# Kernel optimization log

Hardware: AMD Instinct MI355X
Metric: run time of the kernel (lower is better)

Reference implementation:

```python
import jax, jax.numpy as jnp
import numpy as np

E, NL, CH, M1, M2 = 8, 4, 32, 16, 16   # experts, fno layers, hidden channels, fourier modes
HD, NH, NENC = 64, 4, 2                 # router hidden dim, heads, encoder layers
B, CIN, H, W, COUT = 32, 1, 128, 128, 1
PCH = 128                               # projection channels


def _ln(h, s, b):
    mu = h.mean(-1, keepdims=True)
    v = ((h - mu) ** 2).mean(-1, keepdims=True)
    return (h - mu) / jnp.sqrt(v + 1e-5) * s + b


def _router(x, enc_in_w, enc_in_b, qkv_w, qkv_b, ao_w, ao_b,
            ln1_s, ln1_b, ff1_w, ff1_b, ff2_w, ff2_b, ln2_s, ln2_b, fc_w, fc_b):
    ic = x[:, :, 0, :]                                        # (B, C, W): initial condition
    h = jnp.einsum('bcs,cd->bsd', ic, enc_in_w) + enc_in_b    # (B, S, HD)
    S = h.shape[1]
    dh = HD // NH
    for l in range(NENC):  # small fixed layer count
        qkv = h @ qkv_w[l] + qkv_b[l]
        q, k, v = jnp.split(qkv, 3, axis=-1)
        q = q.reshape(-1, S, NH, dh)
        k = k.reshape(-1, S, NH, dh)
        v = v.reshape(-1, S, NH, dh)
        att = jax.nn.softmax(jnp.einsum('bqhd,bkhd->bhqk', q, k) / np.float32(np.sqrt(dh)), axis=-1)
        o = jnp.einsum('bhqk,bkhd->bqhd', att, v).reshape(-1, S, HD)
        h = _ln(h + o @ ao_w[l] + ao_b[l], ln1_s[l], ln1_b[l])
        ff = jax.nn.relu(h @ ff1_w[l] + ff1_b[l]) @ ff2_w[l] + ff2_b[l]
        h = _ln(h + ff, ln2_s[l], ln2_b[l])
    feats = h.mean(axis=1)                                    # (B, HD)
    logits = feats @ fc_w + fc_b                              # (B, E)
    return jnp.argmax(logits, axis=-1), logits                # hard routing (eval path)


def _fno(x, idx, lift_w, lift_b, spec_wr, spec_wi, skip_w, skip_b, p1_w, p1_b, p2_w, p2_b):
    # Hard-MoE dispatch/combine expressed as per-sample expert-weight gather:
    # mathematically identical to running each sample through its selected expert.
    v = jnp.einsum('bchw,bcd->bdhw', x, lift_w[idx]) + lift_b[idx][:, :, None, None]
    for l in range(NL):
        Wc = spec_wr[idx, l] + 1j * spec_wi[idx, l]           # (B,2,CH,CH,M1,M2) complex
        X = jnp.fft.rfft2(v)                                  # (B,CH,H,W//2+1)
        o1 = jnp.einsum('bixy,bioxy->boxy', X[:, :, :M1, :M2], Wc[:, 0])
        o2 = jnp.einsum('bixy,bioxy->boxy', X[:, :, -M1:, :M2], Wc[:, 1])
        out_ft = jnp.zeros(X.shape, X.dtype).at[:, :, :M1, :M2].set(o1).at[:, :, -M1:, :M2].set(o2)
        spec = jnp.fft.irfft2(out_ft, s=(v.shape[-2], v.shape[-1]))
        skip = jnp.einsum('bihw,bio->bohw', v, skip_w[idx, l]) + skip_b[idx, l][:, :, None, None]
        v = spec + skip
        if l < NL - 1:
            v = jax.nn.gelu(v)
    h = jax.nn.gelu(jnp.einsum('bihw,bio->bohw', v, p1_w[idx]) + p1_b[idx][:, :, None, None])
    return jnp.einsum('bihw,bio->bohw', h, p2_w[idx]) + p2_b[idx][:, :, None, None]


def setup_inputs() -> dict:
    key = jax.random.key(0)
    ks = iter(jax.random.split(key, 40))
    def rn(shape, scale=1.0):
        return jax.random.normal(next(ks), shape, jnp.float32) * scale
    return {
        'x': rn((B, CIN, H, W)),
        'enc_in_w': rn((CIN, HD)), 'enc_in_b': jnp.zeros((HD,), jnp.float32),
        'qkv_w': rn((NENC, HD, 3 * HD), HD ** -0.5), 'qkv_b': jnp.zeros((NENC, 3 * HD), jnp.float32),
        'ao_w': rn((NENC, HD, HD), HD ** -0.5), 'ao_b': jnp.zeros((NENC, HD), jnp.float32),
        'ln1_s': jnp.ones((NENC, HD), jnp.float32), 'ln1_b': jnp.zeros((NENC, HD), jnp.float32),
        'ff1_w': rn((NENC, HD, 4 * HD), HD ** -0.5), 'ff1_b': jnp.zeros((NENC, 4 * HD), jnp.float32),
        'ff2_w': rn((NENC, 4 * HD, HD), (4 * HD) ** -0.5), 'ff2_b': jnp.zeros((NENC, HD), jnp.float32),
        'ln2_s': jnp.ones((NENC, HD), jnp.float32), 'ln2_b': jnp.zeros((NENC, HD), jnp.float32),
        'fc_w': rn((HD, E), HD ** -0.5), 'fc_b': jnp.zeros((E,), jnp.float32),
        'lift_w': rn((E, CIN, CH)), 'lift_b': jnp.zeros((E, CH), jnp.float32),
        'spec_wr': rn((E, NL, 2, CH, CH, M1, M2), 1.0 / CH),
        'spec_wi': rn((E, NL, 2, CH, CH, M1, M2), 1.0 / CH),
        'skip_w': rn((E, NL, CH, CH), CH ** -0.5), 'skip_b': jnp.zeros((E, NL, CH), jnp.float32),
        'p1_w': rn((E, CH, PCH), CH ** -0.5), 'p1_b': jnp.zeros((E, PCH), jnp.float32),
        'p2_w': rn((E, PCH, COUT), PCH ** -0.5), 'p2_b': jnp.zeros((E, COUT), jnp.float32),
    }


def reference(x, enc_in_w, enc_in_b, qkv_w, qkv_b, ao_w, ao_b, ln1_s, ln1_b,
              ff1_w, ff1_b, ff2_w, ff2_b, ln2_s, ln2_b, fc_w, fc_b,
              lift_w, lift_b, spec_wr, spec_wi, skip_w, skip_b, p1_w, p1_b, p2_w, p2_b):
    idx, _ = _router(x, enc_in_w, enc_in_b, qkv_w, qkv_b, ao_w, ao_b,
                     ln1_s, ln1_b, ff1_w, ff1_b, ff2_w, ff2_b, ln2_s, ln2_b, fc_w, fc_b)
    return _fno(x, idx, lift_w, lift_b, spec_wr, spec_wi, skip_w, skip_b, p1_w, p1_b, p2_w, p2_b)
```

## Files before the change

kernel.cpp:

```cpp
#include <hip/hip_runtime.h>
#include <hip/hip_bf16.h>
#include <math.h>

typedef __attribute__((ext_vector_type(8))) short bf16x8;
typedef __attribute__((ext_vector_type(4))) float f32x4;
typedef __attribute__((ext_vector_type(2))) float f32x2;

__device__ __forceinline__ float gelu_f(float x){
    float u = 0.7978845608028654f*(x + 0.044715f*x*x*x);
    float e = __expf(2.0f*u);
    float th = 1.0f - 2.0f/(e + 1.0f);
    return 0.5f*x*(1.0f + th);
}

__device__ __forceinline__ short f2bs(float f){
    unsigned u = __float_as_uint(f);
    u += 0x7FFF + ((u>>16)&1);
    return (short)(u>>16);
}

__global__ void r_embed(const float* __restrict__ x, const float* __restrict__ ew,
                        const float* __restrict__ eb, float* __restrict__ h){
    int t = blockIdx.x*256 + threadIdx.x;
    int d = t & 63, s = (t>>6)&127, b = t>>13;
    h[t] = x[b*16384 + s]*ew[d] + eb[d];
}

__global__ void r_qkv(const float* __restrict__ h, const float* __restrict__ w,
                      const float* __restrict__ bias, int woff, int boff,
                      float* __restrict__ qkv){
    int t = blockIdx.x*256 + threadIdx.x;
    int j = t % 192; int sb = t/192;
    const float* hr = h + sb*64;
    float acc = bias[boff + j];
    #pragma unroll
    for(int d=0; d<64; ++d) acc += hr[d]*w[woff + d*192 + j];
    qkv[t] = acc;
}

__global__ __launch_bounds__(128) void r_attn(const float* __restrict__ qkv,
                                              float* __restrict__ o){
    __shared__ float Ks[128][16];
    __shared__ float Vs[128][16];
    int b  = blockIdx.x >> 2;
    int hd = blockIdx.x & 3;
    int q  = threadIdx.x;
    const float* base = qkv + b*128*192;
    {
        const float* kr = base + q*192 + 64  + hd*16;
        const float* vr = base + q*192 + 128 + hd*16;
        #pragma unroll
        for(int j=0;j<4;++j){
            *(float4*)&Ks[q][4*j] = *(const float4*)(kr + 4*j);
            *(float4*)&Vs[q][4*j] = *(const float4*)(vr + 4*j);
        }
    }
    float qv[16];
    {
        const float* qr = base + q*192 + hd*16;
        #pragma unroll
        for(int d=0;d<16;++d) qv[d] = qr[d];
    }
    __syncthreads();
    float m = -1e30f;
    #pragma unroll 4
    for(int k=0;k<128;++k){
        float acc=0.f;
        #pragma unroll
        for(int d=0;d<16;++d) acc += qv[d]*Ks[k][d];
        m = fmaxf(m, acc*0.25f);
    }
    float sum=0.f; float ov[16];
    #pragma unroll
    for(int d=0;d<16;++d) ov[d]=0.f;
    #pragma unroll 2
    for(int k=0;k<128;++k){
        float acc=0.f;
        #pragma unroll
        for(int d=0;d<16;++d) acc += qv[d]*Ks[k][d];
        float p = __expf(acc*0.25f - m); sum += p;
        #pragma unroll
        for(int d=0;d<16;++d) ov[d] += p*Vs[k][d];
    }
    float inv = 1.0f/sum;
    float* orow = o + (b*128+q)*64 + hd*16;
    #pragma unroll
    for(int d=0;d<16;++d) orow[d] = ov[d]*inv;
}

__global__ void r_proj_res(const float* __restrict__ h, const float* __restrict__ o,
                           const float* __restrict__ w, const float* __restrict__ bias,
                           int woff, int boff, float* __restrict__ r){
    int t = blockIdx.x*256 + threadIdx.x;
    int d = t & 63; int sb = t>>6;
    const float* orow = o + sb*64;
    float acc = bias[boff + d];
    #pragma unroll
    for(int e=0;e<64;++e) acc += orow[e]*w[woff + e*64 + d];
    r[t] = h[t] + acc;
}

__global__ void r_ln(const float* __restrict__ r, const float* __restrict__ s,
                     const float* __restrict__ bias, int off, float* __restrict__ h){
    int row = blockIdx.x*64 + threadIdx.x;
    const float* rr = r + row*64;
    float mu=0.f;
    #pragma unroll
    for(int d=0;d<64;++d) mu += rr[d];
    mu *= (1.0f/64.0f);
    float var=0.f;
    #pragma unroll
    for(int d=0;d<64;++d){ float df = rr[d]-mu; var += df*df; }
    var *= (1.0f/64.0f);
    float inv = rsqrtf(var + 1e-5f);
    float* hr = h + row*64;
    #pragma unroll
    for(int d=0;d<64;++d) hr[d] = (rr[d]-mu)*inv*s[off+d] + bias[off+d];
}

__global__ void r_ffn(const float* __restrict__ h, const float* __restrict__ w1,
                      const float* __restrict__ b1, const float* __restrict__ w2,
                      const float* __restrict__ b2,
                      int w1off, int b1off, int w2off, int b2off,
                      float* __restrict__ r){
    __shared__ float hrow[64];
    __shared__ float uval[256];
    int row = blockIdx.x;
    int tid = threadIdx.x;
    if(tid < 64) hrow[tid] = h[row*64 + tid];
    __syncthreads();
    {
        float acc = b1[b1off + tid];
        #pragma unroll
        for(int d=0; d<64; ++d) acc += hrow[d]*w1[w1off + d*256 + tid];
        uval[tid] = fmaxf(acc, 0.0f);
    }
    __syncthreads();
    if(tid < 64){
        float acc = b2[b2off + tid];
        for(int j=0;j<256;++j) acc += uval[j]*w2[w2off + j*64 + tid];
        r[row*64 + tid] = hrow[tid] + acc;
    }
}

__global__ void r_head(const float* __restrict__ h, const float* __restrict__ fcw,
                       const float* __restrict__ fcb, int* __restrict__ idx){
    __shared__ float feats[64];
    __shared__ float lg[8];
    int b = blockIdx.x; int d = threadIdx.x;
    float acc=0.f;
    for(int s2=0;s2<128;++s2) acc += h[(b*128+s2)*64 + d];
    feats[d] = acc*(1.0f/128.0f);
    __syncthreads();
    if(d<8){
        float a = fcb[d];
        for(int e=0;e<64;++e) a += feats[e]*fcw[e*8+d];
        lg[d]=a;
    }
    __syncthreads();
    if(d==0){
        int best=0; float bv=lg[0];
        for(int e=1;e<8;++e) if(lg[e]>bv){bv=lg[e];best=e;}
        idx[b]=best;
    }
}

__global__ void f_lift(const float* __restrict__ x, const float* __restrict__ lw,
                       const float* __restrict__ lb, const int* __restrict__ idx,
                       int b0, float* __restrict__ v){
    int t = blockIdx.x*256 + threadIdx.x;
    int w = t & 127; int h2 = (t>>7)&127; int d = (t>>14)&31; int bl = t>>19;
    int b = b0 + bl;
    int e = idx[b];
    v[t] = x[b*16384 + h2*128 + w]*lw[e*32+d] + lb[e*32+d];
}

__global__ __launch_bounds__(256) void f_fwd(const float* __restrict__ v,
                                             float* __restrict__ G){
    __shared__ float cT[128], sT[128];
    __shared__ float X[2*16*260 + 8];
    int tid = threadIdx.x;
    if(tid<128){ float sv,cv; __sincosf(6.283185307179586f*tid/128.0f,&sv,&cv); cT[tid]=cv; sT[tid]=sv; }
    __syncthreads();
    int bi0 = blockIdx.x*2;
    {
        int bil = tid>>7, h = tid&127;
        const float* row = v + ((bi0+bil)*128 + h)*128;
        float Xr[16], Xi[16];
        #pragma unroll
        for(int k=0;k<16;++k){ Xr[k]=0.f; Xi[k]=0.f; }
        #pragma unroll
        for(int j=0;j<8;++j){
            float4 a = *(const float4*)(row + 4*j);
            float4 bq= *(const float4*)(row + 4*j + 32);
            float4 c = *(const float4*)(row + 4*j + 64);
            float4 dq= *(const float4*)(row + 4*j + 96);
            #pragma unroll
            for(int r=0;r<4;++r){
                int g = 4*j + r;
                float va = (r==0)?a.x:(r==1)?a.y:(r==2)?a.z:a.w;
                float vb = (r==0)?bq.x:(r==1)?bq.y:(r==2)?bq.z:bq.w;
                float vc = (r==0)?c.x:(r==1)?c.y:(r==2)?c.z:c.w;
                float vd = (r==0)?dq.x:(r==1)?dq.y:(r==2)?dq.z:dq.w;
                float s1=va+vc, s2=vb+vd, d1=va-vc, d2=vb-vd;
                float rsum=s1+s2, rdif=s1-s2;
                float pc=cT[g], ps=-sT[g];
                float cr=1.f, ci=0.f;
                #pragma unroll
                for(int ky=0;ky<16;++ky){
                    int mm = ky&3;
                    if(mm==0){ Xr[ky]+=cr*rsum; Xi[ky]+=ci*rsum; }
                    else if(mm==1){ Xr[ky]+=cr*d1+ci*d2; Xi[ky]+=ci*d1-cr*d2; }
                    else if(mm==2){ Xr[ky]+=cr*rdif; Xi[ky]+=ci*rdif; }
                    else { Xr[ky]+=cr*d1-ci*d2; Xi[ky]+=ci*d1+cr*d2; }
                    float tt=cr*pc-ci*ps; ci=cr*ps+ci*pc; cr=tt;
                }
            }
        }
        float* Xb = X + bil*4160;
        #pragma unroll
        for(int ky=0;ky<16;++ky){
            Xb[ky*260 + h*2]   = Xr[ky];
            Xb[ky*260 + h*2+1] = Xi[ky];
        }
    }
    __syncthreads();
    {
        int ky = tid&15, kg = (tid>>4)&7, bil = tid>>7;
        int bi = bi0 + bil;
        const float* Xb = X + bil*4160 + ky*260;
        int kxs[4] = {kg, kg+8, kg+112, kg+120};
        float qc[4], qs[4];
        #pragma unroll
        for(int m2=0;m2<4;++m2){ qc[m2]=cT[kxs[m2]&127]; qs[m2]=-sT[kxs[m2]&127]; }
        float cr[4]={1.f,1.f,1.f,1.f}, ci[4]={0.f,0.f,0.f,0.f};
        float Gr[4]={0.f,0.f,0.f,0.f}, Gi[4]={0.f,0.f,0.f,0.f};
        for(int h=0;h<128;++h){
            float Xr=Xb[h*2], Xi2=Xb[h*2+1];
            #pragma unroll
            for(int m2=0;m2<4;++m2){
                Gr[m2] += Xr*cr[m2] - Xi2*ci[m2];
                Gi[m2] += Xr*ci[m2] + Xi2*cr[m2];
                float t=cr[m2]*qc[m2]-ci[m2]*qs[m2]; ci[m2]=cr[m2]*qs[m2]+ci[m2]*qc[m2]; cr[m2]=t;
            }
        }
        #pragma unroll
        for(int m2=0;m2<4;++m2){
            int kxi = kg + 8*m2;
            G[((bi*32+kxi)*16+ky)*2]   = Gr[m2];
            G[((bi*32+kxi)*16+ky)*2+1] = Gi[m2];
        }
    }
}

__global__ void f_specmul(const float* __restrict__ G, const float* __restrict__ wr,
                          const float* __restrict__ wi, const int* __restrict__ idx,
                          int l, int b0, float* __restrict__ Go){
    int t = blockIdx.x*256 + threadIdx.x;
    int ky = t & 15; int kxi = (t>>4)&31; int o = (t>>9)&31; int bl = t>>14;
    int e = __builtin_amdgcn_readfirstlane(idx[b0 + bl]);
    int side = (kxi>=16) ? 1 : 0; int xm = kxi & 15;
    int wbase = ((((e*4+l)*2+side)*32)*32 + o)*256 + xm*16 + ky;
    const float* gp = G + ((bl*1024 + kxi)*16 + ky)*2;
    float orr=0.f, oii=0.f;
    #pragma unroll 8
    for(int i=0;i<32;++i){
        float gr = gp[i*1024], gi = gp[i*1024+1];
        float wrv = wr[wbase + i*8192];
        float wiv = wi[wbase + i*8192];
        orr += gr*wrv - gi*wiv;
        oii += gr*wiv + gi*wrv;
    }
    Go[t*2]=orr; Go[t*2+1]=oii;
}

__global__ __launch_bounds__(128) void f_idft_h(const float* __restrict__ Go,
                                                float* __restrict__ T){
    __shared__ float cT[128], sT[128];
    int tid = threadIdx.x;
    { float sv,cv; __sincosf(6.283185307179586f*tid/128.0f,&sv,&cv); cT[tid]=cv; sT[tid]=sv; }
    __syncthreads();
    int bo = blockIdx.x;
    const float* g = Go + bo*1024;
    int h = tid;
    float Mc = cT[h], Ms = sT[h];
    float Tr[16], Ti[16];
    #pragma unroll
    for(int k=0;k<16;++k){ Tr[k]=0.f; Ti[k]=0.f; }
    {   float cr=1.f, ci=0.f;
        for(int kxi=0;kxi<16;++kxi){
            #pragma unroll
            for(int ky=0;ky<16;++ky){
                float gr=g[(kxi*16+ky)*2], gi=g[(kxi*16+ky)*2+1];
                Tr[ky] += gr*cr - gi*ci;
                Ti[ky] += gr*ci + gi*cr;
            }
            float t=cr*Mc-ci*Ms; ci=cr*Ms+ci*Mc; cr=t;
        }
    }
    {   float cr=1.f, ci=0.f;
        for(int m=1;m<=16;++m){
            float t=cr*Mc+ci*Ms; ci=ci*Mc-cr*Ms; cr=t;
            int kxi = 32 - m;
            #pragma unroll
            for(int ky=0;ky<16;++ky){
                float gr=g[(kxi*16+ky)*2], gi=g[(kxi*16+ky)*2+1];
                Tr[ky] += gr*cr - gi*ci;
                Ti[ky] += gr*ci + gi*cr;
            }
        }
    }
    float* out = T + (bo*128 + h)*32;
    #pragma unroll
    for(int k=0;k<8;++k){
        *(float4*)(out + 4*k) = make_float4(Tr[2*k], Ti[2*k], Tr[2*k+1], Ti[2*k+1]);
    }
}

__global__ __launch_bounds__(128) void f_inv_w_skip(const float* __restrict__ T,
                             float* __restrict__ v,
                             const float* __restrict__ skw, const float* __restrict__ skb,
                             const int* __restrict__ idx, int l, int act, int b0){
    __shared__ float Tl[1024];
    __shared__ float Wl[1024];
    int tid = threadIdx.x;
    int bl = blockIdx.x >> 7; int h2 = blockIdx.x & 127;
    int e = __builtin_amdgcn_readfirstlane(idx[b0 + bl]);
    int w = tid;
    const float* swp = skw + (e*4+l)*1024;
    const float* sbp = skb + (e*4+l)*32;
    {
        #pragma unroll
        for(int rep=0; rep<2; ++rep){
            int g = rep*512 + tid*4;
            int o = g>>5, j = g&31;
            *(float4*)&Tl[g] = *(const float4*)(T + ((bl*32+o)*128 + h2)*32 + j);
        }
        int gi = tid>>2, go = (tid&3)*8;
        float4 wa = *(const float4*)(swp + gi*32 + go);
        float4 wb = *(const float4*)(swp + gi*32 + go + 4);
        Wl[(go+0)*32+gi]=wa.x; Wl[(go+1)*32+gi]=wa.y;
        Wl[(go+2)*32+gi]=wa.z; Wl[(go+3)*32+gi]=wa.w;
        Wl[(go+4)*32+gi]=wb.x; Wl[(go+5)*32+gi]=wb.y;
        Wl[(go+6)*32+gi]=wb.z; Wl[(go+7)*32+gi]=wb.w;
    }
    f32x2 vv[16];
    #pragma unroll
    for(int i=0;i<16;++i){
        float lo = v[((bl*32+2*i  )*128+h2)*128 + w];
        float hi = v[((bl*32+2*i+1)*128+h2)*128 + w];
        vv[i].x = lo; vv[i].y = hi;
    }
    f32x2 CS[16];
    {
        float bs, bc; __sincosf(6.283185307179586f*w/128.0f, &bs, &bc);
        float cr=bc, ci=bs;
        CS[0].x = 1.f; CS[0].y = 0.f;
        #pragma unroll
        for(int ky=1;ky<16;++ky){
            CS[ky].x = 2.f*cr; CS[ky].y = -2.f*ci;
            float t2=cr*bc-ci*bs; ci=cr*bs+ci*bc; cr=t2;
        }
    }
    __syncthreads();
    #pragma unroll 1
    for(int o=0;o<32;o+=2){
        const f32x2* W0 = (const f32x2*)&Wl[o*32];
        const f32x2* W1 = (const f32x2*)&Wl[o*32+32];
        const f32x2* T0 = (const f32x2*)&Tl[o*32];
        const f32x2* T1 = (const f32x2*)&Tl[o*32+32];
        f32x2 a  = {0.f,0.f}, a2 = {0.f,0.f};
        f32x2 b  = {0.f,0.f}, b2 = {0.f,0.f};
        f32x2 s  = {0.f,0.f}, s2 = {0.f,0.f};
        f32x2 t  = {0.f,0.f}, t2 = {0.f,0.f};
        #pragma unroll
        for(int k=0;k<16;k+=2){
            a  = vv[k]  *W0[k]   + a;
            a2 = vv[k+1]*W0[k+1] + a2;
            b  = vv[k]  *W1[k]   + b;
            b2 = vv[k+1]*W1[k+1] + b2;
            s  = T0[k]  *CS[k]   + s;
            s2 = T0[k+1]*CS[k+1] + s2;
            t  = T1[k]  *CS[k]   + t;
            t2 = T1[k+1]*CS[k+1] + t2;
        }
        float skip0 = sbp[o]   + ((a.x+a.y)+(a2.x+a2.y));
        float skip1 = sbp[o+1] + ((b.x+b.y)+(b2.x+b2.y));
        float spec0 = (s.x+s.y)+(s2.x+s2.y);
        float spec1 = (t.x+t.y)+(t2.x+t2.y);
        float val0 = spec0*(1.0f/16384.0f) + skip0;
        float val1 = spec1*(1.0f/16384.0f) + skip1;
        if(act){ val0 = gelu_f(val0); val1 = gelu_f(val1); }
        v[((bl*32+o  )*128+h2)*128 + w] = val0;
        v[((bl*32+o+1)*128+h2)*128 + w] = val1;
    }
}

__global__ __launch_bounds__(256) void f_proj(const float* __restrict__ vin,
                       const float* __restrict__ p1w, const float* __restrict__ p1b,
                       const float* __restrict__ p2w, const float* __restrict__ p2b,
                       const int* __restrict__ idx, int b0, float* __restrict__ out){
    int tid = threadIdx.x;
    int wv  = tid>>6, lane = tid&63;
    int blk = blockIdx.x;
    int bl  = blk>>5; int part = blk&31;
    int b   = b0 + bl;
    int e   = __builtin_amdgcn_readfirstlane(idx[b]);
    int m   = lane&15, quad = lane>>4;
    const float* w1 = p1w + e*4096;
    bf16x8 bfr[8]; float b1v[8], w2v[8];
    #pragma unroll
    for(int og=0; og<8; ++og){
        int o = og*16 + m;
        #pragma unroll
        for(int j=0;j<8;++j){
            int k = quad*8 + j;
            bfr[og][j] = f2bs(w1[k*128 + o]);
        }
        b1v[og] = p1b[e*128+o];
        w2v[og] = p2w[e*128+o];
    }
    float p2bv = p2b[e];
    const float* vbase = vin + (size_t)bl*524288;
    for(int t=0;t<8;++t){
        int tile = part*32 + wv*8 + t;
        int pix0 = tile*16;
        bf16x8 af;
        #pragma unroll
        for(int j=0;j<8;++j){
            int k = quad*8 + j;
            af[j] = f2bs(vbase[k*16384 + pix0 + m]);
        }
        float acc0=0.f, acc1=0.f, acc2=0.f, acc3=0.f;
        #pragma unroll
        for(int og=0;og<8;++og){
            f32x4 d = {0.f,0.f,0.f,0.f};
            d = __builtin_amdgcn_mfma_f32_16x16x32_bf16(af, bfr[og], d, 0,0,0);
            acc0 += w2v[og]*gelu_f(d[0]+b1v[og]);
            acc1 += w2v[og]*gelu_f(d[1]+b1v[og]);
            acc2 += w2v[og]*gelu_f(d[2]+b1v[og]);
            acc3 += w2v[og]*gelu_f(d[3]+b1v[og]);
        }
        #pragma unroll
        for(int s=1;s<16;s<<=1){
            acc0 += __shfl_xor(acc0, s, 64);
            acc1 += __shfl_xor(acc1, s, 64);
            acc2 += __shfl_xor(acc2, s, 64);
            acc3 += __shfl_xor(acc3, s, 64);
        }
        if(m==0){
            int pix = pix0 + quad*4;
            *(float4*)(out + (size_t)b*16384 + pix) =
                make_float4(acc0+p2bv, acc1+p2bv, acc2+p2bv, acc3+p2bv);
        }
    }
}

extern "C" void kernel_launch(void* const* d_in, const int* in_sizes, int n_in,
                              void* d_out, int out_size, void* d_ws, size_t ws_size,
                              hipStream_t stream){
    const float* x      = (const float*)d_in[0];
    const float* enc_w  = (const float*)d_in[1];
    const float* enc_b  = (const float*)d_in[2];
    const float* qkv_w  = (const float*)d_in[3];
    const float* qkv_b  = (const float*)d_in[4];
    const float* ao_w   = (const float*)d_in[5];
    const float* ao_b   = (const float*)d_in[6];
    const float* ln1_s  = (const float*)d_in[7];
    const float* ln1_b  = (const float*)d_in[8];
    const float* ff1_w  = (const float*)d_in[9];
    const float* ff1_b  = (const float*)d_in[10];
    const float* ff2_w  = (const float*)d_in[11];
    const float* ff2_b  = (const float*)d_in[12];
    const float* ln2_s  = (const float*)d_in[13];
    const float* ln2_b  = (const float*)d_in[14];
    const float* fc_w   = (const float*)d_in[15];
    const float* fc_b   = (const float*)d_in[16];
    const float* lift_w = (const float*)d_in[17];
    const float* lift_b = (const float*)d_in[18];
    const float* spec_wr= (const float*)d_in[19];
    const float* spec_wi= (const float*)d_in[20];
    const float* skip_w = (const float*)d_in[21];
    const float* skip_b = (const float*)d_in[22];
    const float* p1_w   = (const float*)d_in[23];
    const float* p1_b   = (const float*)d_in[24];
    const float* p2_w   = (const float*)d_in[25];
    const float* p2_b   = (const float*)d_in[26];

    int*   idx   = (int*)d_ws + 8;
    float* base  = (float*)d_ws + 64;

    size_t avail_fl = (ws_size/4 > 64) ? (ws_size/4 - 64) : 0;
    int nb = 1;
    for(int c = 32; c >= 1; c >>= 1){
        if((size_t)c*851968 <= avail_fl){ nb = c; break; }
    }

    float* hbuf  = base;
    float* qkvb  = hbuf + 262144;
    float* obuf  = qkvb + 786432;
    float* rbuf  = obuf + 262144;

    r_embed<<<1024,256,0,stream>>>(x, enc_w, enc_b, hbuf);
    for(int l=0;l<2;++l){
        r_qkv<<<3072,256,0,stream>>>(hbuf, qkv_w, qkv_b, l*64*192, l*192, qkvb);
        r_attn<<<128,128,0,stream>>>(qkvb, obuf);
        r_proj_res<<<1024,256,0,stream>>>(hbuf, obuf, ao_w, ao_b, l*64*64, l*64, rbuf);
        r_ln<<<64,64,0,stream>>>(rbuf, ln1_s, ln1_b, l*64, hbuf);
        r_ffn<<<4096,256,0,stream>>>(hbuf, ff1_w, ff1_b, ff2_w, ff2_b,
                                     l*64*256, l*256, l*256*64, l*64, rbuf);
        r_ln<<<64,64,0,stream>>>(rbuf, ln2_s, ln2_b, l*64, hbuf);
    }
    r_head<<<32,64,0,stream>>>(hbuf, fc_w, fc_b, idx);

    for(int b0 = 0; b0 < 32; b0 += nb){
        float* vC = base;
        float* G  = vC + (size_t)nb*655360;
        float* Go = G  + (size_t)nb*32768;
        float* T  = Go + (size_t)nb*32768;

        f_lift<<<nb*2048,256,0,stream>>>(x, lift_w, lift_b, idx, b0, vC);
        for(int l=0;l<4;++l){
            f_fwd    <<<nb*16, 256,0,stream>>>(vC, G);
            f_specmul<<<nb*64, 256,0,stream>>>(G, spec_wr, spec_wi, idx, l, b0, Go);
            f_idft_h <<<nb*32, 128,0,stream>>>(Go, T);
            f_inv_w_skip<<<nb*128,128,0,stream>>>(T, vC, skip_w, skip_b, idx,
                                                  l, (l<3)?1:0, b0);
        }
        f_proj<<<nb*32,256,0,stream>>>(vC, p1_w, p1_b, p2_w, p2_b, idx, b0,
                                       (float*)d_out);
    }
}
```

Baseline: 1.023 ms.

## Compute first-layer spectrum from single-channel input and scale by lift weights

The lift is a per-channel affine map of a single input channel, so the first layer's truncated Fourier transform equals the input's transform scaled per channel, with the bias added only to the DC mode. The first layer now runs one DFT per sample on the raw input (f_fwd_x), then a cheap scaling kernel, instead of transforming all 32 lifted channels. This removes most of the first-layer forward DFT work. In exchange it adds a launch, assumes CIN equals 1, and introduces a second DFT code path that must match f_fwd's mode ordering and scaling.

```diff
diff --git a/kernel.cpp b/kernel.cpp
--- a/kernel.cpp
+++ b/kernel.cpp
@@ -251,6 +251,97 @@
             G[((bi*32+kxi)*16+ky)*2+1] = Gi[m2];
         }
     }
+}
+
+__global__ __launch_bounds__(256) void f_fwd_x(const float* __restrict__ x,
+                                               int b0, float* __restrict__ Gx){
+    __shared__ float cT[128], sT[128];
+    __shared__ float X[16*260 + 8];
+    int tid = threadIdx.x;
+    if(tid<128){ float sv,cv; __sincosf(6.283185307179586f*tid/128.0f,&sv,&cv); cT[tid]=cv; sT[tid]=sv; }
+    __syncthreads();
+    int bl = blockIdx.x;
+    {
+        int kyg = tid>>7, h = tid&127;
+        int ky0 = kyg*8;
+        const float* row = x + (b0+bl)*16384 + h*128;
+        float Xr[8], Xi[8];
+        #pragma unroll
+        for(int k=0;k<8;++k){ Xr[k]=0.f; Xi[k]=0.f; }
+        #pragma unroll
+        for(int j=0;j<8;++j){
+            float4 a = *(const float4*)(row + 4*j);
+            float4 bq= *(const float4*)(row + 4*j + 32);
+            float4 c = *(const float4*)(row + 4*j + 64);
+            float4 dq= *(const float4*)(row + 4*j + 96);
+            #pragma unroll
+            for(int r=0;r<4;++r){
+                int g = 4*j + r;
+                float va = (r==0)?a.x:(r==1)?a.y:(r==2)?a.z:a.w;
+                float vb = (r==0)?bq.x:(r==1)?bq.y:(r==2)?bq.z:bq.w;
+                float vc = (r==0)?c.x:(r==1)?c.y:(r==2)?c.z:c.w;
+                float vd = (r==0)?dq.x:(r==1)?dq.y:(r==2)?dq.z:dq.w;
+                float s1=va+vc, s2=vb+vd, d1=va-vc, d2=vb-vd;
+                float rsum=s1+s2, rdif=s1-s2;
+                float pc=cT[g], ps=-sT[g];
+                int p0 = (g*ky0)&127;
+                float cr=cT[p0], ci=-sT[p0];
+                #pragma unroll
+                for(int ky=0;ky<8;++ky){
+                    int mm = ky&3;
+                    if(mm==0){ Xr[ky]+=cr*rsum; Xi[ky]+=ci*rsum; }
+                    else if(mm==1){ Xr[ky]+=cr*d1+ci*d2; Xi[ky]+=ci*d1-cr*d2; }
+                    else if(mm==2){ Xr[ky]+=cr*rdif; Xi[ky]+=ci*rdif; }
+                    else { Xr[ky]+=cr*d1-ci*d2; Xi[ky]+=ci*d1+cr*d2; }
+                    float tt=cr*pc-ci*ps; ci=cr*ps+ci*pc; cr=tt;
+                }
+            }
+        }
+        #pragma unroll
+        for(int ky=0;ky<8;++ky){
+            X[(ky0+ky)*260 + h*2]   = Xr[ky];
+            X[(ky0+ky)*260 + h*2+1] = Xi[ky];
+        }
+    }
+    __syncthreads();
+    {
+        int ky = tid&15, kg = tid>>4;
+        const float* Xb = X + ky*260;
+        int kxa[2] = {kg, kg+112};
+        float qc[2], qs[2];
+        #pragma unroll
+        for(int m2=0;m2<2;++m2){ qc[m2]=cT[kxa[m2]&127]; qs[m2]=-sT[kxa[m2]&127]; }
+        float cr[2]={1.f,1.f}, ci[2]={0.f,0.f};
+        float Gr[2]={0.f,0.f}, Gi[2]={0.f,0.f};
+        for(int h=0;h<128;++h){
+            float Xr=Xb[h*2], Xi2=Xb[h*2+1];
+            #pragma unroll
+            for(int m2=0;m2<2;++m2){
+                Gr[m2] += Xr*cr[m2] - Xi2*ci[m2];
+                Gi[m2] += Xr*ci[m2] + Xi2*cr[m2];
+                float t=cr[m2]*qc[m2]-ci[m2]*qs[m2]; ci[m2]=cr[m2]*qs[m2]+ci[m2]*qc[m2]; cr[m2]=t;
+            }
+        }
+        #pragma unroll
+        for(int m2=0;m2<2;++m2){
+            int store = kg + 16*m2;
+            Gx[bl*1024 + (store*16+ky)*2]   = Gr[m2];
+            Gx[bl*1024 + (store*16+ky)*2+1] = Gi[m2];
+        }
+    }
+}
+
+__global__ void f_scale(const float* __restrict__ Gx, const float* __restrict__ lw,
+                        const float* __restrict__ lb, const int* __restrict__ idx,
+                        int b0, float* __restrict__ G){
+    int t = blockIdx.x*256 + threadIdx.x;
+    int p = t & 511; int d = (t>>9)&31; int bl = t>>14;
+    int e = idx[b0 + bl];
+    float a = lw[e*32+d];
+    float gr = Gx[bl*1024 + p*2], gi = Gx[bl*1024 + p*2+1];
+    float orr = a*gr, oii = a*gi;
+    if(p==0) orr += lb[e*32+d]*16384.0f;
+    G[t*2] = orr; G[t*2+1] = oii;
 }
 
 __global__ void f_specmul(const float* __restrict__ G, const float* __restrict__ wr,
@@ -515,13 +606,19 @@
 
     for(int b0 = 0; b0 < 32; b0 += nb){
         float* vC = base;
+        float* Gx = vC + (size_t)nb*524288;
         float* G  = vC + (size_t)nb*655360;
         float* Go = G  + (size_t)nb*32768;
         float* T  = Go + (size_t)nb*32768;
 
         f_lift<<<nb*2048,256,0,stream>>>(x, lift_w, lift_b, idx, b0, vC);
         for(int l=0;l<4;++l){
-            f_fwd    <<<nb*16, 256,0,stream>>>(vC, G);
+            if(l==0){
+                f_fwd_x<<<nb,   256,0,stream>>>(x, b0, Gx);
+                f_scale<<<nb*64,256,0,stream>>>(Gx, lift_w, lift_b, idx, b0, G);
+            }else{
+                f_fwd  <<<nb*16,256,0,stream>>>(vC, G);
+            }
             f_specmul<<<nb*64, 256,0,stream>>>(G, spec_wr, spec_wi, idx, l, b0, Go);
             f_idft_h <<<nb*32, 128,0,stream>>>(Go, T);
             f_inv_w_skip<<<nb*128,128,0,stream>>>(T, vC, skip_w, skip_b, idx,
```

Result: faster. 973.3 us (-4.9%).
